# Kernel tuning notes

Hardware: AMD Instinct MI355X
Metric: run time of the kernel (lower is better)

The kernel has to match this reference:

```python
import jax, jax.numpy as jnp
import numpy as np

T, B, H, E, V = 128, 64, 512, 256, 32000
UNK = 2
EPS = 1e-10


def setup_inputs() -> dict:
    key = jax.random.key(0)
    ks = jax.random.split(key, 16)
    s = 0.02
    return {
        "u_enc_out": jax.random.normal(ks[0], (T, B, H), jnp.float32),
        "z_tm1": jax.random.randint(ks[1], (1, B), 0, V),
        "last_hidden": jax.random.normal(ks[2], (1, B, H), jnp.float32),
        "u_input": jax.random.randint(ks[3], (T, B), 0, V),
        "emb": jax.random.normal(ks[4], (V, E), jnp.float32) * s,
        "attn_W": jax.random.normal(ks[5], (H, 2 * H), jnp.float32) * s,
        "attn_b": jnp.zeros((H,), jnp.float32),
        "attn_v": jax.random.normal(ks[6], (H,), jnp.float32) * (1.0 / np.sqrt(H)),
        "gru_Wih": jax.random.normal(ks[7], (3 * H, H + E), jnp.float32) * s,
        "gru_Whh": jax.random.normal(ks[8], (3 * H, H), jnp.float32) * s,
        "gru_bih": jnp.zeros((3 * H,), jnp.float32),
        "gru_bhh": jnp.zeros((3 * H,), jnp.float32),
        "proj_W": jax.random.normal(ks[9], (V, 2 * H), jnp.float32) * s,
        "proj_b": jnp.zeros((V,), jnp.float32),
        "copy1_W": jax.random.normal(ks[10], (H, H), jnp.float32) * s,
        "copy1_b": jnp.zeros((H,), jnp.float32),
    }


def _copy_logscore(raw, u_input):
    # raw: [B,T] copy scores; u_input: [T,B] int ids
    # Faithful to: log(bmm(exp(raw - max), sparse_one_hot_with_1e-10_floor)) + max
    cmax = jnp.max(raw, axis=1, keepdims=True)            # [B,1]
    ex = jnp.exp(raw - cmax)                              # [B,T]
    idx = u_input.T                                       # [B,T]
    idx = jnp.where(idx == UNK, V + jnp.arange(T)[None, :], idx)
    mask = (u_input.T != 0).astype(ex.dtype)
    total = jnp.sum(ex, axis=1)                           # [B] (all t, incl. ignored)
    scat = jax.vmap(lambda e, i: jnp.zeros((V + T,), ex.dtype).at[i].add(e))(ex * mask, idx)
    return jnp.log(EPS * total[:, None] + (1.0 - EPS) * scat) + cmax  # [B,V+T]


def reference(u_enc_out, z_tm1, last_hidden, u_input, emb, attn_W, attn_b, attn_v,
              gru_Wih, gru_Whh, gru_bih, gru_bhh, proj_W, proj_b, copy1_W, copy1_b):
    enc = jnp.transpose(u_enc_out, (1, 0, 2))             # [B,T,H]
    h = last_hidden[0]                                    # [B,H]
    # Attn: energy = tanh(Linear([h;enc])), score = v . energy, softmax over T
    Hrep = jnp.broadcast_to(h[:, None, :], enc.shape)
    energy = jnp.tanh(jnp.einsum('bti,hi->bth', jnp.concatenate([Hrep, enc], -1), attn_W) + attn_b)
    alpha = jax.nn.softmax(jnp.einsum('h,bth->bt', attn_v, energy), axis=1)
    ctx = jnp.einsum('bt,bth->bh', alpha, enc)            # [B,H]
    # GRU step (pytorch gate order r,z,n)
    x = jnp.concatenate([emb[z_tm1[0]], ctx], axis=-1)    # [B,E+H]
    gi = x @ gru_Wih.T + gru_bih
    gh = h @ gru_Whh.T + gru_bhh
    i_r, i_z, i_n = jnp.split(gi, 3, axis=-1)
    h_r, h_z, h_n = jnp.split(gh, 3, axis=-1)
    r = jax.nn.sigmoid(i_r + h_r)
    z = jax.nn.sigmoid(i_z + h_z)
    n = jnp.tanh(i_n + r * h_n)
    h_new = (1.0 - z) * n + z * h                         # [B,H]
    gru_out = h_new[None]                                 # [1,B,H]
    new_hidden = h_new[None]
    # generation score
    gen_score = jnp.concatenate([h_new, ctx], -1) @ proj_W.T + proj_b  # [B,V]
    # copy score
    cs = jnp.tanh(jnp.einsum('bth,ih->bti', enc, copy1_W) + copy1_b)   # [B,T,H]
    raw = jnp.einsum('bth,bh->bt', cs, h_new)             # [B,T]
    u_copy = _copy_logscore(raw, u_input)                 # [B,V+T]
    scores = jax.nn.softmax(jnp.concatenate([gen_score, u_copy], axis=1), axis=1)
    g, c = scores[:, :V], scores[:, V:]                   # [B,V], [B,V+T]
    proba = jnp.concatenate([g + c[:, :V], c[:, V:]], axis=1)  # [B,V+T]
    return gru_out, new_hidden, proba
```

## Files before the change

### kernel.cpp

```cpp
#include <hip/hip_runtime.h>
#include <math.h>

#define T_ 128
#define B_ 64
#define H_ 512
#define E_ 256
#define V_ 32000
#define VT_ (V_ + T_)
#define UNK_ 2
#define EPS_ 1e-10f
#define NP_ (V_ / 64)

typedef __attribute__((ext_vector_type(8))) _Float16 half8;
typedef __attribute__((ext_vector_type(4))) float floatx4;

#define NB_ZERO 32
#define NB_CVTE 2048
#define NB_CVTA 512
#define NB_CVTC 512
#define NB_WH   8192
#define NB_CVTW 2048
#define NB_XE   64
#define NB_XH   128
#define NB_BC   8
#define NB_PRO (NB_ZERO + NB_CVTE + NB_CVTA + NB_CVTC + NB_WH + NB_CVTW + NB_XE + NB_XH + NB_BC)

__global__ __launch_bounds__(256) void prologue_k(
        const float* __restrict__ u_enc, const float* __restrict__ attn_W,
        const float* __restrict__ copy1_W, const float* __restrict__ last_h,
        const float* __restrict__ attn_b, const float* __restrict__ emb,
        const int* __restrict__ z, const float* __restrict__ Wih,
        const float* __restrict__ Whh, const float* __restrict__ bih,
        const float* __restrict__ bhh,
        float* __restrict__ zbase, _Float16* __restrict__ enc_h,
        _Float16* __restrict__ Wb_attn, _Float16* __restrict__ Wb_copy,
        float* __restrict__ Wh, _Float16* __restrict__ Wcat,
        _Float16* __restrict__ xg, float* __restrict__ bcat) {
    int bid = blockIdx.x, tid = threadIdx.x;
    if (bid < NB_ZERO) { zbase[bid * 256 + tid] = 0.f; return; }
    bid -= NB_ZERO;
    if (bid < NB_CVTE) {
        int i = (bid * 256 + tid) * 8;
        float4 a = *(const float4*)(u_enc + i);
        float4 b = *(const float4*)(u_enc + i + 4);
        half8 o;
        o[0] = (_Float16)a.x; o[1] = (_Float16)a.y; o[2] = (_Float16)a.z; o[3] = (_Float16)a.w;
        o[4] = (_Float16)b.x; o[5] = (_Float16)b.y; o[6] = (_Float16)b.z; o[7] = (_Float16)b.w;
        *(half8*)(enc_h + i) = o;
        return;
    }
    bid -= NB_CVTE;
    if (bid < NB_CVTA) {
        int c = tid * 2;
        float2 v = *(const float2*)(attn_W + (size_t)bid * 1024 + 512 + c);
        Wb_attn[bid * 512 + c]     = (_Float16)v.x;
        Wb_attn[bid * 512 + c + 1] = (_Float16)v.y;
        return;
    }
    bid -= NB_CVTA;
    if (bid < NB_CVTC) {
        int c = tid * 2;
        float2 v = *(const float2*)(copy1_W + (size_t)bid * 512 + c);
        Wb_copy[bid * 512 + c]     = (_Float16)v.x;
        Wb_copy[bid * 512 + c + 1] = (_Float16)v.y;
        return;
    }
    bid -= NB_CVTC;
    if (bid < NB_WH) {
        int wid = bid * 4 + (tid >> 6), lane = tid & 63;
        int b = wid >> 9, m = wid & 511;
        const float4* wr = (const float4*)(attn_W + (size_t)m * 1024);
        const float4* xr = (const float4*)(last_h + b * 512);
        float s = 0.f;
        #pragma unroll
        for (int i = 0; i < 2; ++i) {
            int k = lane + i * 64;
            float4 w = wr[k], x = xr[k];
            s += w.x * x.x + w.y * x.y + w.z * x.z + w.w * x.w;
        }
        #pragma unroll
        for (int off = 32; off > 0; off >>= 1) s += __shfl_down(s, off);
        if (lane == 0) Wh[b * 512 + m] = s + attn_b[m];
        return;
    }
    bid -= NB_WH;
    if (bid < NB_CVTW) {
        int m = bid;
        #pragma unroll
        for (int j = 0; j < 5; ++j) {
            int c = j * 256 + tid;
            float w;
            if (m < 1024)      w = (c < 768) ? Wih[(size_t)m * 768 + c]
                                             : Whh[(size_t)m * 512 + (c - 768)];
            else if (m < 1536) w = (c < 768) ? Wih[(size_t)m * 768 + c] : 0.f;
            else               w = (c >= 768) ? Whh[(size_t)(m - 512) * 512 + (c - 768)] : 0.f;
            Wcat[(size_t)m * 1280 + c] = (_Float16)w;
        }
        return;
    }
    bid -= NB_CVTW;
    if (bid < NB_XE) {
        int idx = bid * 256 + tid;
        int bb = idx >> 8, c = idx & 255;
        xg[bb * 1280 + c] = (_Float16)emb[(size_t)z[bb] * E_ + c];
        return;
    }
    bid -= NB_XE;
    if (bid < NB_XH) {
        int idx = bid * 256 + tid;
        int bb = idx >> 9, c = idx & 511;
        xg[bb * 1280 + 768 + c] = (_Float16)last_h[bb * H_ + c];
        return;
    }
    bid -= NB_XH;
    {
        int m = bid * 256 + tid;
        float v2;
        if (m < 1024)      v2 = bih[m] + bhh[m];
        else if (m < 1536) v2 = bih[m];
        else               v2 = bhh[m - 512];
        bcat[m] = v2;
    }
}

__global__ __launch_bounds__(256) void enc_dual_k(
        const _Float16* __restrict__ enc_h,
        const _Float16* __restrict__ Wa,
        const _Float16* __restrict__ Wc,
        const float* __restrict__ Wh,
        const float* __restrict__ attn_v,
        const float* __restrict__ copy1_b,
        float* __restrict__ score,
        _Float16* __restrict__ cs) {
    int lane = threadIdx.x & 63;
    int wave = threadIdx.x >> 6;
    int r0 = blockIdx.x * 64;
    int b  = r0 / T_;
    int t0 = r0 % T_;
    int n0 = blockIdx.y * 64 + wave * 16;
    int coln = lane & 15;
    int kq   = (lane >> 4) * 8;
    const _Float16* wra = Wa + (size_t)(n0 + coln) * H_ + kq;
    const _Float16* wrc = Wc + (size_t)(n0 + coln) * H_ + kq;
    floatx4 acca[4] = {}, accc[4] = {};
    #pragma unroll 4
    for (int k0 = 0; k0 < H_; k0 += 32) {
        half8 fba = *(const half8*)(wra + k0);
        half8 fbc = *(const half8*)(wrc + k0);
        #pragma unroll
        for (int mi = 0; mi < 4; ++mi) {
            const _Float16* arow = enc_h +
                ((size_t)(t0 + mi * 16 + coln) * B_ + b) * H_ + k0 + kq;
            half8 fa = *(const half8*)arow;
            acca[mi] = __builtin_amdgcn_mfma_f32_16x16x32_f16(fa, fba, acca[mi], 0, 0, 0);
            accc[mi] = __builtin_amdgcn_mfma_f32_16x16x32_f16(fa, fbc, accc[mi], 0, 0, 0);
        }
    }
    int col = n0 + coln;
    float addt = Wh[b * H_ + col];
    float av   = attn_v[col];
    float cb   = copy1_b[col];
    int rbase = (lane >> 4) * 4;
    #pragma unroll
    for (int mi = 0; mi < 4; ++mi)
        #pragma unroll
        for (int r = 0; r < 4; ++r) {
            int row = r0 + mi * 16 + rbase + r;
            float x = acca[mi][r] + addt;
            float t2 = __expf(2.f * x);
            float v = av * ((t2 - 1.f) / (t2 + 1.f));
            v += __shfl_xor(v, 1);
            v += __shfl_xor(v, 2);
            v += __shfl_xor(v, 4);
            v += __shfl_xor(v, 8);
            if (coln == 0) atomicAdd(&score[row], v);
            float y = accc[mi][r] + cb;
            float t3 = __expf(2.f * y);
            cs[(size_t)row * H_ + col] = (_Float16)((t3 - 1.f) / (t3 + 1.f));
        }
}

__global__ __launch_bounds__(256) void softctx_k(
        const float* __restrict__ score, const float* __restrict__ u_enc,
        _Float16* __restrict__ xcat, _Float16* __restrict__ xg) {
    __shared__ float al[T_];
    __shared__ float red[T_];
    int b = blockIdx.x, tid = threadIdx.x;
    float v = (tid < T_) ? score[b * T_ + tid] : -1e30f;
    if (tid < T_) red[tid] = v;
    __syncthreads();
    for (int s = 64; s > 0; s >>= 1) { if (tid < s) red[tid] = fmaxf(red[tid], red[tid + s]); __syncthreads(); }
    float m = red[0]; __syncthreads();
    float e = (tid < T_) ? __expf(v - m) : 0.f;
    if (tid < T_) red[tid] = e;
    __syncthreads();
    for (int s = 64; s > 0; s >>= 1) { if (tid < s) red[tid] += red[tid + s]; __syncthreads(); }
    if (tid < T_) al[tid] = e / red[0];
    __syncthreads();
    int h = blockIdx.y * 256 + tid;
    float s2 = 0.f;
    #pragma unroll 4
    for (int t = 0; t < T_; ++t) s2 += al[t] * u_enc[((size_t)t * B_ + b) * H_ + h];
    xcat[b * 1024 + 512 + h] = (_Float16)s2;
    xg[b * 1280 + 256 + h]   = (_Float16)s2;
}

__global__ __launch_bounds__(256) void grucat_k(
        const _Float16* __restrict__ xg,
        const _Float16* __restrict__ Wcat,
        const float* __restrict__ bcat,
        float* __restrict__ S) {
    int lane = threadIdx.x & 63;
    int wave = threadIdx.x >> 6;
    int n0 = (blockIdx.x * 4 + wave) * 16;
    int coln = lane & 15;
    int kq  = (lane >> 4) * 8;
    const _Float16* wrow = Wcat + (size_t)(n0 + coln) * 1280 + kq;
    const _Float16* abase = xg + kq;
    floatx4 acc[4] = {};
    #pragma unroll 8
    for (int k0 = 0; k0 < 1280; k0 += 32) {
        half8 fb = *(const half8*)(wrow + k0);
        #pragma unroll
        for (int mi = 0; mi < 4; ++mi) {
            half8 fa = *(const half8*)(abase + (size_t)(mi * 16 + coln) * 1280 + k0);
            acc[mi] = __builtin_amdgcn_mfma_f32_16x16x32_f16(fa, fb, acc[mi], 0, 0, 0);
        }
    }
    int rbase = (lane >> 4) * 4;
    float bias = bcat[n0 + coln];
    #pragma unroll
    for (int mi = 0; mi < 4; ++mi)
        #pragma unroll
        for (int r = 0; r < 4; ++r)
            S[(size_t)(mi * 16 + rbase + r) * 2048 + n0 + coln] = acc[mi][r] + bias;
}

__global__ void gru_k(const float* __restrict__ S, const float* __restrict__ hprev,
                      float* __restrict__ out, _Float16* __restrict__ xcat) {
    int b = blockIdx.x;
    int m = blockIdx.y * 256 + threadIdx.x;
    float r  = 1.f / (1.f + __expf(-S[b * 2048 + m]));
    float zz = 1.f / (1.f + __expf(-S[b * 2048 + 512 + m]));
    float n  = tanhf(S[b * 2048 + 1024 + m] + r * S[b * 2048 + 1536 + m]);
    float h = hprev[b * H_ + m];
    float hv = (1.f - zz) * n + zz * h;
    out[b * H_ + m] = hv;
    out[B_ * H_ + b * H_ + m] = hv;
    xcat[b * 1024 + m] = (_Float16)hv;
}

__global__ __launch_bounds__(256) void proj_stats_k(
        const _Float16* __restrict__ xcat,
        const float* __restrict__ Wp,
        const float* __restrict__ bp,
        float* __restrict__ gen,
        float* __restrict__ mpart, float* __restrict__ lpart) {
    __shared__ float m_lds[4][64];
    __shared__ float l_lds[4][64];
    int lane = threadIdx.x & 63;
    int wave = threadIdx.x >> 6;
    int n0 = (blockIdx.x * 4 + wave) * 16;
    int coln = lane & 15;
    int kq  = (lane >> 4) * 8;
    const float* wrow = Wp + (size_t)(n0 + coln) * 1024 + kq;
    const _Float16* abase = xcat + kq;
    floatx4 acc[4] = {};
    #pragma unroll 8
    for (int k0 = 0; k0 < 1024; k0 += 32) {
        const float4* wb = (const float4*)(wrow + k0);
        float4 w0 = wb[0], w1 = wb[1];
        half8 fb;
        fb[0] = (_Float16)w0.x; fb[1] = (_Float16)w0.y; fb[2] = (_Float16)w0.z; fb[3] = (_Float16)w0.w;
        fb[4] = (_Float16)w1.x; fb[5] = (_Float16)w1.y; fb[6] = (_Float16)w1.z; fb[7] = (_Float16)w1.w;
        #pragma unroll
        for (int mi = 0; mi < 4; ++mi) {
            half8 fa = *(const half8*)(abase + (size_t)(mi * 16 + coln) * 1024 + k0);
            acc[mi] = __builtin_amdgcn_mfma_f32_16x16x32_f16(fa, fb, acc[mi], 0, 0, 0);
        }
    }
    int rbase = (lane >> 4) * 4;
    float bias = bp[n0 + coln];
    #pragma unroll
    for (int mi = 0; mi < 4; ++mi)
        #pragma unroll
        for (int r = 0; r < 4; ++r) {
            int brow = mi * 16 + rbase + r;
            float x = acc[mi][r] + bias;
            gen[(size_t)brow * V_ + n0 + coln] = x;
            float mm = x;
            mm = fmaxf(mm, __shfl_xor(mm, 1));
            mm = fmaxf(mm, __shfl_xor(mm, 2));
            mm = fmaxf(mm, __shfl_xor(mm, 4));
            mm = fmaxf(mm, __shfl_xor(mm, 8));
            float e = __expf(x - mm);
            e += __shfl_xor(e, 1);
            e += __shfl_xor(e, 2);
            e += __shfl_xor(e, 4);
            e += __shfl_xor(e, 8);
            if (coln == 0) { m_lds[wave][brow] = mm; l_lds[wave][brow] = e; }
        }
    __syncthreads();
    if (threadIdx.x < 64) {
        int bb = threadIdx.x;
        float M = m_lds[0][bb], L = l_lds[0][bb];
        #pragma unroll
        for (int w = 1; w < 4; ++w) {
            float m2 = m_lds[w][bb], l2 = l_lds[w][bb];
            float nm = fmaxf(M, m2);
            L = L * __expf(M - nm) + l2 * __expf(m2 - nm);
            M = nm;
        }
        mpart[bb * NP_ + blockIdx.x] = M;
        lpart[bb * NP_ + blockIdx.x] = L;
    }
}

__global__ __launch_bounds__(256) void raw_epi_k(
        const _Float16* __restrict__ cs, const float* __restrict__ hnew,
        const int* __restrict__ u_input, float* __restrict__ scat,
        float* __restrict__ sc4) {
    __shared__ float rawS[T_];
    __shared__ float red[T_];
    int b = blockIdx.x, tid = threadIdx.x;
    int lane = tid & 63, wave = tid >> 6;
    const float4* hp = (const float4*)(hnew + b * H_ + lane * 8);
    float4 ha = hp[0], hb = hp[1];
    #pragma unroll 4
    for (int i = 0; i < 32; ++i) {
        int t = wave * 32 + i;
        half8 c8 = *(const half8*)(cs + (size_t)(b * T_ + t) * H_ + lane * 8);
        float s = (float)c8[0] * ha.x + (float)c8[1] * ha.y + (float)c8[2] * ha.z + (float)c8[3] * ha.w
                + (float)c8[4] * hb.x + (float)c8[5] * hb.y + (float)c8[6] * hb.z + (float)c8[7] * hb.w;
        #pragma unroll
        for (int off = 32; off > 0; off >>= 1) s += __shfl_down(s, off);
        if (lane == 0) rawS[t] = s;
    }
    __syncthreads();
    int t = tid;
    float v = (t < T_) ? rawS[t] : -1e30f;
    if (t < T_) red[t] = v;
    __syncthreads();
    for (int s = 64; s > 0; s >>= 1) { if (t < s) red[t] = fmaxf(red[t], red[t + s]); __syncthreads(); }
    float cm = red[0]; __syncthreads();
    float e = (t < T_) ? __expf(v - cm) : 0.f;
    if (t < T_) red[t] = e;
    __syncthreads();
    for (int s = 64; s > 0; s >>= 1) { if (t < s) red[t] += red[t + s]; __syncthreads(); }
    float tot = red[0]; __syncthreads();
    int id = (t < T_) ? u_input[t * B_ + b] : 0;
    size_t j = (size_t)b * VT_ + ((id == UNK_) ? (V_ + t) : id);
    if (id != 0) scat[j] = 0.f;
    __syncthreads();
    if (id != 0) atomicAdd(&scat[j], e);
    if (t < T_) red[t] = (id != 0) ? e : 0.f;
    __syncthreads();
    for (int s = 64; s > 0; s >>= 1) { if (t < s) red[t] += red[t + s]; __syncthreads(); }
    float ssum = red[0]; __syncthreads();
    float sv = (id != 0) ? scat[j] : 0.f;
    if (t < T_) red[t] = sv;
    __syncthreads();
    for (int s = 64; s > 0; s >>= 1) { if (t < s) red[t] = fmaxf(red[t], red[t + s]); __syncthreads(); }
    if (t == 0) {
        sc4[b * 4 + 0] = cm;
        sc4[b * 4 + 1] = tot;
        sc4[b * 4 + 2] = ssum;
        sc4[b * 4 + 3] = red[0];
    }
}

__global__ void combine_k(const float* __restrict__ mpart, const float* __restrict__ lpart,
                          const float* __restrict__ sc4, float* __restrict__ params) {
    __shared__ float ms[256], ls[256];
    int b = blockIdx.x, tid = threadIdx.x;
    float M = -1e30f, L = 0.f;
    for (int s = tid; s < NP_; s += 256) {
        float m2 = mpart[b * NP_ + s], l2 = lpart[b * NP_ + s];
        float nm = fmaxf(M, m2);
        L = L * __expf(M - nm) + l2 * __expf(m2 - nm);
        M = nm;
    }
    ms[tid] = M; ls[tid] = L;
    __syncthreads();
    for (int s = 128; s > 0; s >>= 1) {
        if (tid < s) {
            float m2 = ms[tid + s], l2 = ls[tid + s];
            float nm = fmaxf(ms[tid], m2);
            ls[tid] = ls[tid] * __expf(ms[tid] - nm) + l2 * __expf(m2 - nm);
            ms[tid] = nm;
        }
        __syncthreads();
    }
    if (tid == 0) {
        float Mg = ms[0], Zg = ls[0];
        float cm = sc4[b * 4], tot = sc4[b * 4 + 1], ssum = sc4[b * 4 + 2], smax = sc4[b * 4 + 3];
        float umax = cm + logf(EPS_ * tot + (1.f - EPS_) * smax);
        float M2 = fmaxf(Mg, umax);
        float coef = __expf(cm - M2);
        float Z = Zg * __expf(Mg - M2) + coef * (EPS_ * tot * (float)VT_ + (1.f - EPS_) * ssum);
        float invZ = 1.f / Z;
        params[b * 4 + 0] = M2;
        params[b * 4 + 1] = invZ;
        params[b * 4 + 2] = coef * EPS_ * tot * invZ;
        params[b * 4 + 3] = coef * (1.f - EPS_) * invZ;
    }
}

__global__ __launch_bounds__(256) void write_k(const float* __restrict__ gen,
                                               const float* __restrict__ params,
                                               float* __restrict__ proba) {
    int b = blockIdx.y;
    int i4 = blockIdx.x * 256 + threadIdx.x;
    if (i4 >= VT_ / 4) return;
    float M = params[b * 4], invZ = params[b * 4 + 1], addc = params[b * 4 + 2];
    int j = i4 * 4;
    float4 p;
    if (j < V_) {
        float4 g = *(const float4*)(gen + (size_t)b * V_ + j);
        p.x = addc + __expf(g.x - M) * invZ;
        p.y = addc + __expf(g.y - M) * invZ;
        p.z = addc + __expf(g.z - M) * invZ;
        p.w = addc + __expf(g.w - M) * invZ;
    } else {
        p.x = p.y = p.z = p.w = addc;
    }
    *(float4*)(proba + (size_t)b * VT_ + j) = p;
}

__global__ void fix_k(const float* __restrict__ gen, const float* __restrict__ scat,
                      const int* __restrict__ u_input, const float* __restrict__ params,
                      float* __restrict__ proba) {
    int b = blockIdx.x, t = threadIdx.x;
    int id = u_input[t * B_ + b];
    if (id == 0) return;
    int j = (id == UNK_) ? (V_ + t) : id;
    float M = params[b * 4], invZ = params[b * 4 + 1];
    float addc = params[b * 4 + 2], scoef = params[b * 4 + 3];
    float p = addc + scoef * scat[(size_t)b * VT_ + j];
    if (j < V_) p += __expf(gen[(size_t)b * V_ + j] - M) * invZ;
    proba[(size_t)b * VT_ + j] = p;
}

extern "C" void kernel_launch(void* const* d_in, const int* in_sizes, int n_in,
                              void* d_out, int out_size, void* d_ws, size_t ws_size,
                              hipStream_t stream) {
    const float* u_enc   = (const float*)d_in[0];
    const int*   z_tm1   = (const int*)d_in[1];
    const float* last_h  = (const float*)d_in[2];
    const int*   u_input = (const int*)d_in[3];
    const float* emb     = (const float*)d_in[4];
    const float* attn_W  = (const float*)d_in[5];
    const float* attn_b  = (const float*)d_in[6];
    const float* attn_v  = (const float*)d_in[7];
    const float* gru_Wih = (const float*)d_in[8];
    const float* gru_Whh = (const float*)d_in[9];
    const float* gru_bih = (const float*)d_in[10];
    const float* gru_bhh = (const float*)d_in[11];
    const float* proj_W  = (const float*)d_in[12];
    const float* proj_b  = (const float*)d_in[13];
    const float* copy1_W = (const float*)d_in[14];
    const float* copy1_b = (const float*)d_in[15];
    float* out = (float*)d_out;

    float* ws    = (float*)d_ws;
    float* score = ws;
    float* gen   = score + B_ * T_;
    float* scat  = gen + (size_t)B_ * V_;
    float* Wh    = scat + (size_t)B_ * VT_;
    float* S     = Wh + B_ * H_;
    float* sc4   = S + B_ * 2048;
    float* mpart = sc4 + B_ * 4;
    float* lpart = mpart + B_ * NP_;
    float* params= lpart + B_ * NP_;
    float* bcat  = params + B_ * 4;
    _Float16* xcat  = (_Float16*)(bcat + 2048);
    _Float16* xg    = xcat + B_ * 1024;
    _Float16* enc_h = xg + B_ * 1280;
    _Float16* Wb_attn = enc_h + (size_t)T_ * B_ * H_;
    _Float16* Wb_copy = Wb_attn + H_ * H_;
    _Float16* Wcat  = Wb_copy + H_ * H_;
    _Float16* cs    = Wcat + 2048 * 1280;

    prologue_k<<<NB_PRO, 256, 0, stream>>>(u_enc, attn_W, copy1_W, last_h, attn_b,
                                           emb, z_tm1, gru_Wih, gru_Whh, gru_bih, gru_bhh,
                                           score, enc_h, Wb_attn, Wb_copy, Wh, Wcat, xg, bcat);

    dim3 g2(T_ * B_ / 64, H_ / 64);
    enc_dual_k<<<g2, 256, 0, stream>>>(enc_h, Wb_attn, Wb_copy, Wh, attn_v, copy1_b,
                                       score, cs);

    softctx_k<<<dim3(B_, 2), 256, 0, stream>>>(score, u_enc, xcat, xg);

    grucat_k<<<2048 / 64, 256, 0, stream>>>(xg, Wcat, bcat, S);

    gru_k<<<dim3(B_, 2), 256, 0, stream>>>(S, last_h, out, xcat);

    proj_stats_k<<<NP_, 256, 0, stream>>>(xcat, proj_W, proj_b, gen, mpart, lpart);

    raw_epi_k<<<B_, 256, 0, stream>>>(cs, out, u_input, scat, sc4);

    combine_k<<<B_, 256, 0, stream>>>(mpart, lpart, sc4, params);

    float* proba = out + 2 * B_ * H_;
    write_k<<<dim3((VT_ / 4 + 255) / 256, B_), 256, 0, stream>>>(gen, params, proba);
    fix_k<<<B_, T_, 0, stream>>>(gen, scat, u_input, params, proba);
}
```

Measured before the change: 395.9 us.

## Fuse GRU gates into GEMM epilogue, merge combine into raw_epi, read fp16 encoder

Result: no change. 393.2 us (-0.7%).

```diff
diff --git a/kernel.cpp b/kernel.cpp
--- a/kernel.cpp
+++ b/kernel.cpp
@@ -85,16 +85,20 @@
     }
     bid -= NB_WH;
     if (bid < NB_CVTW) {
-        int m = bid;
+        int mp = bid;
+        int q  = (mp >> 4) & 3;
+        int hh = (mp >> 6) * 16 + (mp & 15);
         #pragma unroll
         for (int j = 0; j < 5; ++j) {
             int c = j * 256 + tid;
             float w;
-            if (m < 1024)      w = (c < 768) ? Wih[(size_t)m * 768 + c]
-                                             : Whh[(size_t)m * 512 + (c - 768)];
-            else if (m < 1536) w = (c < 768) ? Wih[(size_t)m * 768 + c] : 0.f;
-            else               w = (c >= 768) ? Whh[(size_t)(m - 512) * 512 + (c - 768)] : 0.f;
-            Wcat[(size_t)m * 1280 + c] = (_Float16)w;
+            if (q == 0)      w = (c < 768) ? Wih[(size_t)hh * 768 + c]
+                                           : Whh[(size_t)hh * 512 + (c - 768)];
+            else if (q == 1) w = (c < 768) ? Wih[(size_t)(512 + hh) * 768 + c]
+                                           : Whh[(size_t)(512 + hh) * 512 + (c - 768)];
+            else if (q == 2) w = (c < 768) ? Wih[(size_t)(1024 + hh) * 768 + c] : 0.f;
+            else             w = (c >= 768) ? Whh[(size_t)(1024 + hh) * 512 + (c - 768)] : 0.f;
+            Wcat[(size_t)mp * 1280 + c] = (_Float16)w;
         }
         return;
     }
@@ -114,12 +118,15 @@
     }
     bid -= NB_XH;
     {
-        int m = bid * 256 + tid;
+        int mp = bid * 256 + tid;
+        int q  = (mp >> 4) & 3;
+        int hh = (mp >> 6) * 16 + (mp & 15);
         float v2;
-        if (m < 1024)      v2 = bih[m] + bhh[m];
-        else if (m < 1536) v2 = bih[m];
-        else               v2 = bhh[m - 512];
-        bcat[m] = v2;
+        if (q == 0)      v2 = bih[hh] + bhh[hh];
+        else if (q == 1) v2 = bih[512 + hh] + bhh[512 + hh];
+        else if (q == 2) v2 = bih[1024 + hh];
+        else             v2 = bhh[1024 + hh];
+        bcat[mp] = v2;
     }
 }
 
@@ -181,7 +188,7 @@
 }
 
 __global__ __launch_bounds__(256) void softctx_k(
-        const float* __restrict__ score, const float* __restrict__ u_enc,
+        const float* __restrict__ score, const _Float16* __restrict__ enc_h,
         _Float16* __restrict__ xcat, _Float16* __restrict__ xg) {
     __shared__ float al[T_];
     __shared__ float red[T_];
@@ -200,7 +207,7 @@
     int h = blockIdx.y * 256 + tid;
     float s2 = 0.f;
     #pragma unroll 4
-    for (int t = 0; t < T_; ++t) s2 += al[t] * u_enc[((size_t)t * B_ + b) * H_ + h];
+    for (int t = 0; t < T_; ++t) s2 += al[t] * (float)enc_h[((size_t)t * B_ + b) * H_ + h];
     xcat[b * 1024 + 512 + h] = (_Float16)s2;
     xg[b * 1280 + 256 + h]   = (_Float16)s2;
 }
@@ -209,10 +216,13 @@
         const _Float16* __restrict__ xg,
         const _Float16* __restrict__ Wcat,
         const float* __restrict__ bcat,
-        float* __restrict__ S) {
+        const float* __restrict__ hprev,
+        float* __restrict__ out,
+        _Float16* __restrict__ xcat) {
+    __shared__ float Lt[4][64][16];
     int lane = threadIdx.x & 63;
     int wave = threadIdx.x >> 6;
-    int n0 = (blockIdx.x * 4 + wave) * 16;
+    int n0 = blockIdx.x * 64 + wave * 16;
     int coln = lane & 15;
     int kq  = (lane >> 4) * 8;
     const _Float16* wrow = Wcat + (size_t)(n0 + coln) * 1280 + kq;
@@ -233,21 +243,21 @@
     for (int mi = 0; mi < 4; ++mi)
         #pragma unroll
         for (int r = 0; r < 4; ++r)
-            S[(size_t)(mi * 16 + rbase + r) * 2048 + n0 + coln] = acc[mi][r] + bias;
-}
-
-__global__ void gru_k(const float* __restrict__ S, const float* __restrict__ hprev,
-                      float* __restrict__ out, _Float16* __restrict__ xcat) {
-    int b = blockIdx.x;
-    int m = blockIdx.y * 256 + threadIdx.x;
-    float r  = 1.f / (1.f + __expf(-S[b * 2048 + m]));
-    float zz = 1.f / (1.f + __expf(-S[b * 2048 + 512 + m]));
-    float n  = tanhf(S[b * 2048 + 1024 + m] + r * S[b * 2048 + 1536 + m]);
-    float h = hprev[b * H_ + m];
-    float hv = (1.f - zz) * n + zz * h;
-    out[b * H_ + m] = hv;
-    out[B_ * H_ + b * H_ + m] = hv;
-    xcat[b * 1024 + m] = (_Float16)hv;
+            Lt[wave][mi * 16 + rbase + r][coln] = acc[mi][r] + bias;
+    __syncthreads();
+    int HB = blockIdx.x * 16;
+    #pragma unroll
+    for (int p = threadIdx.x; p < 1024; p += 256) {
+        int b = p >> 4, i = p & 15;
+        float rr = 1.f / (1.f + __expf(-Lt[0][b][i]));
+        float zz = 1.f / (1.f + __expf(-Lt[1][b][i]));
+        float nn = tanhf(Lt[2][b][i] + rr * Lt[3][b][i]);
+        float h  = hprev[b * H_ + HB + i];
+        float hv = (1.f - zz) * nn + zz * h;
+        out[b * H_ + HB + i] = hv;
+        out[B_ * H_ + b * H_ + HB + i] = hv;
+        xcat[b * 1024 + HB + i] = (_Float16)hv;
+    }
 }
 
 __global__ __launch_bounds__(256) void proj_stats_k(
@@ -318,10 +328,12 @@
 
 __global__ __launch_bounds__(256) void raw_epi_k(
         const _Float16* __restrict__ cs, const float* __restrict__ hnew,
-        const int* __restrict__ u_input, float* __restrict__ scat,
-        float* __restrict__ sc4) {
+        const int* __restrict__ u_input,
+        const float* __restrict__ mpart, const float* __restrict__ lpart,
+        float* __restrict__ scat, float* __restrict__ params) {
     __shared__ float rawS[T_];
     __shared__ float red[T_];
+    __shared__ float ms[256], ls[256];
     int b = blockIdx.x, tid = threadIdx.x;
     int lane = tid & 63, wave = tid >> 6;
     const float4* hp = (const float4*)(hnew + b * H_ + lane * 8);
@@ -361,39 +373,27 @@
     if (t < T_) red[t] = sv;
     __syncthreads();
     for (int s = 64; s > 0; s >>= 1) { if (t < s) red[t] = fmaxf(red[t], red[t + s]); __syncthreads(); }
-    if (t == 0) {
-        sc4[b * 4 + 0] = cm;
-        sc4[b * 4 + 1] = tot;
-        sc4[b * 4 + 2] = ssum;
-        sc4[b * 4 + 3] = red[0];
-    }
-}
-
-__global__ void combine_k(const float* __restrict__ mpart, const float* __restrict__ lpart,
-                          const float* __restrict__ sc4, float* __restrict__ params) {
-    __shared__ float ms[256], ls[256];
-    int b = blockIdx.x, tid = threadIdx.x;
+    float smax = red[0]; __syncthreads();
     float M = -1e30f, L = 0.f;
-    for (int s = tid; s < NP_; s += 256) {
+    for (int s = t; s < NP_; s += 256) {
         float m2 = mpart[b * NP_ + s], l2 = lpart[b * NP_ + s];
         float nm = fmaxf(M, m2);
         L = L * __expf(M - nm) + l2 * __expf(m2 - nm);
         M = nm;
     }
-    ms[tid] = M; ls[tid] = L;
+    ms[t] = M; ls[t] = L;
     __syncthreads();
     for (int s = 128; s > 0; s >>= 1) {
-        if (tid < s) {
-            float m2 = ms[tid + s], l2 = ls[tid + s];
-            float nm = fmaxf(ms[tid], m2);
-            ls[tid] = ls[tid] * __expf(ms[tid] - nm) + l2 * __expf(m2 - nm);
-            ms[tid] = nm;
+        if (t < s) {
+            float m2 = ms[t + s], l2 = ls[t + s];
+            float nm = fmaxf(ms[t], m2);
+            ls[t] = ls[t] * __expf(ms[t] - nm) + l2 * __expf(m2 - nm);
+            ms[t] = nm;
         }
         __syncthreads();
     }
-    if (tid == 0) {
+    if (t == 0) {
         float Mg = ms[0], Zg = ls[0];
-        float cm = sc4[b * 4], tot = sc4[b * 4 + 1], ssum = sc4[b * 4 + 2], smax = sc4[b * 4 + 3];
         float umax = cm + logf(EPS_ * tot + (1.f - EPS_) * smax);
         float M2 = fmaxf(Mg, umax);
         float coef = __expf(cm - M2);
@@ -467,9 +467,7 @@
     float* gen   = score + B_ * T_;
     float* scat  = gen + (size_t)B_ * V_;
     float* Wh    = scat + (size_t)B_ * VT_;
-    float* S     = Wh + B_ * H_;
-    float* sc4   = S + B_ * 2048;
-    float* mpart = sc4 + B_ * 4;
+    float* mpart = Wh + B_ * H_;
     float* lpart = mpart + B_ * NP_;
     float* params= lpart + B_ * NP_;
     float* bcat  = params + B_ * 4;
@@ -489,17 +487,13 @@
     enc_dual_k<<<g2, 256, 0, stream>>>(enc_h, Wb_attn, Wb_copy, Wh, attn_v, copy1_b,
                                        score, cs);
 
-    softctx_k<<<dim3(B_, 2), 256, 0, stream>>>(score, u_enc, xcat, xg);
-
-    grucat_k<<<2048 / 64, 256, 0, stream>>>(xg, Wcat, bcat, S);
-
-    gru_k<<<dim3(B_, 2), 256, 0, stream>>>(S, last_h, out, xcat);
+    softctx_k<<<dim3(B_, 2), 256, 0, stream>>>(score, enc_h, xcat, xg);
+
+    grucat_k<<<2048 / 64, 256, 0, stream>>>(xg, Wcat, bcat, last_h, out, xcat);
 
     proj_stats_k<<<NP_, 256, 0, stream>>>(xcat, proj_W, proj_b, gen, mpart, lpart);
 
-    raw_epi_k<<<B_, 256, 0, stream>>>(cs, out, u_input, scat, sc4);
-
-    combine_k<<<B_, 256, 0, stream>>>(mpart, lpart, sc4, params);
+    raw_epi_k<<<B_, 256, 0, stream>>>(cs, out, u_input, mpart, lpart, scat, params);
 
     float* proba = out + 2 * B_ * H_;
     write_k<<<dim3((VT_ / 4 + 255) / 256, B_), 256, 0, stream>>>(gen, params, proba);
```
